# Optimization experiments

Hardware: AMD Instinct MI355X
Metric: run time of the kernel (lower is better)

## Reference

```python
import jax, jax.numpy as jnp
import numpy as np

N_NODES = 100000
N_EDGES = 1600000
DK = 32
OUT_DIM = 32


def setup_inputs() -> dict:
    key = jax.random.key(0)
    ks = jax.random.split(key, 7)
    X = jax.random.normal(ks[0], (N_NODES, DK), dtype=jnp.float32)
    K = jax.random.normal(ks[1], (N_NODES, DK), dtype=jnp.float32)
    V = jax.random.normal(ks[2], (N_NODES, DK), dtype=jnp.float32)
    # output projection (nn.Dense(out_dim)) params
    W_o = jax.random.normal(ks[3], (DK, OUT_DIM), dtype=jnp.float32) / np.sqrt(DK)
    b_o = jnp.zeros((OUT_DIM,), dtype=jnp.float32)
    # sparsity descriptor td: edge list, dst sorted so segment ops see sorted ids
    src = jax.random.randint(ks[4], (N_EDGES,), 0, N_NODES, dtype=jnp.int32)
    dst = jnp.sort(jax.random.randint(ks[5], (N_EDGES,), 0, N_NODES, dtype=jnp.int32))
    return {"X": X, "K": K, "V": V, "W_o": W_o, "b_o": b_o,
            "src": src, "dst": dst, "num_seg": N_NODES}


def reference(X, K, V, W_o, b_o, src, dst, num_seg):
    dk = X.shape[-1]
    # per-edge attention logits: <Q[dst], K[src]> / dk  -> (E,)
    scores = jnp.einsum('ed,ed->e', jnp.take(X, dst, axis=0),
                        jnp.take(K, src, axis=0)) / dk
    # segment (per-neighborhood) softmax over edges sharing a dst node
    seg_max = jax.ops.segment_max(scores, dst, num_segments=num_seg,
                                  indices_are_sorted=True)
    e = jnp.exp(scores - jnp.take(seg_max, dst))
    denom = jax.ops.segment_sum(e, dst, num_segments=num_seg,
                                indices_are_sorted=True)
    alpha = e / jnp.take(denom, dst)  # (E,)
    # weighted aggregation of values, scattered back to nodes -> (N, dk)
    agg = jax.ops.segment_sum(alpha[:, None] * jnp.take(V, src, axis=0), dst,
                              num_segments=num_seg, indices_are_sorted=True)
    # output projection W_o
    return agg @ W_o + b_o
```

## Files before the change

### kernel.cpp

```cpp
#include <hip/hip_runtime.h>
#include <math.h>

#define DK 32
#define OUT_DIM 32
#define NODES_PER_WAVE 4

__global__ void build_row_ptr_kernel(const int* __restrict__ dst, int E, int N,
                                     int* __restrict__ row_ptr) {
    int e = blockIdx.x * blockDim.x + threadIdx.x;
    if (e >= E) return;
    int cur  = dst[e];
    int prev = (e == 0) ? -1 : dst[e - 1];
    for (int j = prev + 1; j <= cur; ++j) row_ptr[j] = e;
    if (e == E - 1) {
        for (int j = cur + 1; j <= N; ++j) row_ptr[j] = E;
    }
}

__device__ __forceinline__ unsigned f2bf_rne(float x) {
    unsigned u = __float_as_uint(x);
    return (u + 0x7fffu + ((u >> 16) & 1u)) >> 16;
}

__global__ void repack_kv_kernel(const float* __restrict__ K,
                                 const float* __restrict__ V,
                                 unsigned* __restrict__ KV, int total) {
    int i = blockIdx.x * blockDim.x + threadIdx.x;
    if (i >= total) return;
    KV[i] = (f2bf_rne(V[i]) << 16) | f2bf_rne(K[i]);
}

__global__ __launch_bounds__(256) void gat_node_kv_kernel(
    const float* __restrict__ X, const uint4* __restrict__ KV,
    const float* __restrict__ Wo, const float* __restrict__ bo,
    const int* __restrict__ src, const int* __restrict__ row_ptr,
    float* __restrict__ out, int N) {

    const int tid  = threadIdx.x;
    const int wave = tid >> 6;
    const int lane = tid & 63;
    const int g    = lane >> 3;
    const int c    = lane & 7;
    const int j    = lane & 31;
    const int half = lane >> 5;

    const int n0 = (blockIdx.x * 4 + wave) * NODES_PER_WAVE;
    if (n0 >= N) return;

    float wcol[32];
#pragma unroll
    for (int k = 0; k < 32; ++k) wcol[k] = Wo[k * OUT_DIM + j];
    const float bj = bo[j];

    const float4* X4 = (const float4*)X;

    for (int i = 0; i < NODES_PER_WAVE; ++i) {
        const int n = n0 + i;
        if (n >= N) break;
        const int begin = row_ptr[n];
        const int end   = row_ptr[n + 1];

        float4 q4 = X4[n * 8 + c];
        q4.x *= 0.03125f; q4.y *= 0.03125f;
        q4.z *= 0.03125f; q4.w *= 0.03125f;

        float  l   = 0.0f;
        float4 acc = make_float4(0.0f, 0.0f, 0.0f, 0.0f);

        for (int e0 = begin; e0 < end; e0 += 16) {
            const int  ea = e0 + g;
            const int  eb = ea + 8;
            const int  sa = src[min(ea, end - 1)];
            const int  sb = src[min(eb, end - 1)];
            const uint4 A = KV[sa * 8 + c];
            const uint4 B = KV[sb * 8 + c];

            const float ka0 = __uint_as_float(A.x << 16);
            const float ka1 = __uint_as_float(A.y << 16);
            const float ka2 = __uint_as_float(A.z << 16);
            const float ka3 = __uint_as_float(A.w << 16);
            const float kb0 = __uint_as_float(B.x << 16);
            const float kb1 = __uint_as_float(B.y << 16);
            const float kb2 = __uint_as_float(B.z << 16);
            const float kb3 = __uint_as_float(B.w << 16);

            float pa = fmaf(ka0, q4.x, fmaf(ka1, q4.y, fmaf(ka2, q4.z, ka3 * q4.w)));
            float pb = fmaf(kb0, q4.x, fmaf(kb1, q4.y, fmaf(kb2, q4.z, kb3 * q4.w)));
            pa += __shfl_xor(pa, 1);  pb += __shfl_xor(pb, 1);
            pa += __shfl_xor(pa, 2);  pb += __shfl_xor(pb, 2);
            pa += __shfl_xor(pa, 4);  pb += __shfl_xor(pb, 4);

            const float wa = (ea < end) ? __expf(pa) : 0.0f;
            const float wb = (eb < end) ? __expf(pb) : 0.0f;
            l += wa + wb;

            acc.x = fmaf(wa, __uint_as_float(A.x & 0xffff0000u), acc.x);
            acc.y = fmaf(wa, __uint_as_float(A.y & 0xffff0000u), acc.y);
            acc.z = fmaf(wa, __uint_as_float(A.z & 0xffff0000u), acc.z);
            acc.w = fmaf(wa, __uint_as_float(A.w & 0xffff0000u), acc.w);
            acc.x = fmaf(wb, __uint_as_float(B.x & 0xffff0000u), acc.x);
            acc.y = fmaf(wb, __uint_as_float(B.y & 0xffff0000u), acc.y);
            acc.z = fmaf(wb, __uint_as_float(B.z & 0xffff0000u), acc.z);
            acc.w = fmaf(wb, __uint_as_float(B.w & 0xffff0000u), acc.w);
        }

#pragma unroll
        for (int m = 8; m <= 32; m <<= 1) {
            l     += __shfl_xor(l, m);
            acc.x += __shfl_xor(acc.x, m);
            acc.y += __shfl_xor(acc.y, m);
            acc.z += __shfl_xor(acc.z, m);
            acc.w += __shfl_xor(acc.w, m);
        }

        const float inv = (end > begin) ? (1.0f / l) : 0.0f;

        float ag[4] = {acc.x, acc.y, acc.z, acc.w};
        float s = 0.0f;
#pragma unroll
        for (int k = 0; k < 32; ++k) {
            const float a = __int_as_float(
                __builtin_amdgcn_readlane(__float_as_int(ag[k & 3]), k >> 2));
            s = fmaf(a, wcol[k], s);
        }
        if (half == 0) {
            out[n * OUT_DIM + j] = fmaf(s, inv, bj);
        }
    }
}

__global__ __launch_bounds__(256) void gat_node_f32_kernel(
    const float* __restrict__ X, const float* __restrict__ Km,
    const float* __restrict__ Vm, const float* __restrict__ Wo,
    const float* __restrict__ bo, const int* __restrict__ src,
    const int* __restrict__ row_ptr, float* __restrict__ out, int N) {
    const int tid  = threadIdx.x;
    const int wave = tid >> 6;
    const int lane = tid & 63;
    const int g    = lane >> 3;
    const int c    = lane & 7;
    const int j    = lane & 31;
    const int half = lane >> 5;
    const int n = blockIdx.x * 4 + wave;
    if (n >= N) return;
    const int begin = row_ptr[n];
    const int end   = row_ptr[n + 1];
    const float4* X4 = (const float4*)X;
    const float4* K4 = (const float4*)Km;
    const float4* V4 = (const float4*)Vm;
    const float4 q4 = X4[n * 8 + c];
    float  l   = 0.0f;
    float4 acc = make_float4(0.0f, 0.0f, 0.0f, 0.0f);
    for (int e0 = begin; e0 < end; e0 += 16) {
        const int  ea = e0 + g;
        const int  eb = ea + 8;
        const bool va = ea < end;
        const bool vb = eb < end;
        const int sa = src[min(ea, end - 1)];
        const int sb = src[min(eb, end - 1)];
        const float4 ka  = K4[sa * 8 + c];
        const float4 kb  = K4[sb * 8 + c];
        const float4 vva = V4[sa * 8 + c];
        const float4 vvb = V4[sb * 8 + c];
        float pa = fmaf(ka.x, q4.x, fmaf(ka.y, q4.y, fmaf(ka.z, q4.z, ka.w * q4.w)));
        float pb = fmaf(kb.x, q4.x, fmaf(kb.y, q4.y, fmaf(kb.z, q4.z, kb.w * q4.w)));
        pa += __shfl_xor(pa, 1);  pb += __shfl_xor(pb, 1);
        pa += __shfl_xor(pa, 2);  pb += __shfl_xor(pb, 2);
        pa += __shfl_xor(pa, 4);  pb += __shfl_xor(pb, 4);
        const float wa = va ? __expf(pa * 0.03125f) : 0.0f;
        const float wb = vb ? __expf(pb * 0.03125f) : 0.0f;
        l += wa + wb;
        acc.x = fmaf(wa, vva.x, acc.x);  acc.y = fmaf(wa, vva.y, acc.y);
        acc.z = fmaf(wa, vva.z, acc.z);  acc.w = fmaf(wa, vva.w, acc.w);
        acc.x = fmaf(wb, vvb.x, acc.x);  acc.y = fmaf(wb, vvb.y, acc.y);
        acc.z = fmaf(wb, vvb.z, acc.z);  acc.w = fmaf(wb, vvb.w, acc.w);
    }
#pragma unroll
    for (int m = 8; m <= 32; m <<= 1) {
        l     += __shfl_xor(l, m);
        acc.x += __shfl_xor(acc.x, m);
        acc.y += __shfl_xor(acc.y, m);
        acc.z += __shfl_xor(acc.z, m);
        acc.w += __shfl_xor(acc.w, m);
    }
    const float inv = (end > begin) ? (1.0f / l) : 0.0f;
    float ag[4] = {acc.x, acc.y, acc.z, acc.w};
    float s = 0.0f;
#pragma unroll
    for (int k = 0; k < 32; ++k) {
        const float a = __int_as_float(
            __builtin_amdgcn_readlane(__float_as_int(ag[k & 3]), k >> 2));
        s = fmaf(a, Wo[k * OUT_DIM + j], s);
    }
    if (half == 0) {
        out[n * OUT_DIM + j] = fmaf(s, inv, bo[j]);
    }
}

extern "C" void kernel_launch(void* const* d_in, const int* in_sizes, int n_in,
                              void* d_out, int out_size, void* d_ws, size_t ws_size,
                              hipStream_t stream) {
    const float* X  = (const float*)d_in[0];
    const float* Km = (const float*)d_in[1];
    const float* Vm = (const float*)d_in[2];
    const float* Wo = (const float*)d_in[3];
    const float* bo = (const float*)d_in[4];
    const int* src  = (const int*)d_in[5];
    const int* dst  = (const int*)d_in[6];

    const int N = in_sizes[0] / DK;
    const int E = in_sizes[5];

    int* row_ptr = (int*)d_ws;
    const size_t kv_off = (((size_t)(N + 1) * 4) + 127) & ~(size_t)127;
    unsigned* KV = (unsigned*)((char*)d_ws + kv_off);
    const size_t need = kv_off + (size_t)N * DK * 4;
    float* out = (float*)d_out;

    const int tb = 256;
    build_row_ptr_kernel<<<(E + tb - 1) / tb, tb, 0, stream>>>(dst, E, N, row_ptr);

    if (ws_size >= need) {
        const int total = N * DK;
        repack_kv_kernel<<<(total + tb - 1) / tb, tb, 0, stream>>>(Km, Vm, KV, total);
        const int waves = (N + NODES_PER_WAVE - 1) / NODES_PER_WAVE;
        const int grid  = (waves + 3) / 4;
        gat_node_kv_kernel<<<grid, 256, 0, stream>>>(X, (const uint4*)KV, Wo, bo,
                                                     src, row_ptr, out, N);
    } else {
        const int grid = (N + 3) / 4;
        gat_node_f32_kernel<<<grid, 256, 0, stream>>>(X, Km, Vm, Wo, bo,
                                                      src, row_ptr, out, N);
    }
}
```

Baseline: 157.8 us.

## Batch 16 nodes per wave and do output projection with bf16 MFMA

After: 151.9 us. -3.7%, faster.

```diff
diff --git a/kernel.cpp b/kernel.cpp
--- a/kernel.cpp
+++ b/kernel.cpp
@@ -3,7 +3,9 @@
 
 #define DK 32
 #define OUT_DIM 32
-#define NODES_PER_WAVE 4
+
+typedef float  f32x4  __attribute__((ext_vector_type(4)));
+typedef short  bf16x8 __attribute__((ext_vector_type(8)));
 
 __global__ void build_row_ptr_kernel(const int* __restrict__ dst, int E, int N,
                                      int* __restrict__ row_ptr) {
@@ -30,101 +32,126 @@
     KV[i] = (f2bf_rne(V[i]) << 16) | f2bf_rne(K[i]);
 }
 
-__global__ __launch_bounds__(256) void gat_node_kv_kernel(
+__global__ __launch_bounds__(256) void gat_fused_kernel(
     const float* __restrict__ X, const uint4* __restrict__ KV,
     const float* __restrict__ Wo, const float* __restrict__ bo,
     const int* __restrict__ src, const int* __restrict__ row_ptr,
     float* __restrict__ out, int N) {
+
+    __shared__ uint4 s_part[4][16 * 17];
 
     const int tid  = threadIdx.x;
     const int wave = tid >> 6;
     const int lane = tid & 63;
     const int g    = lane >> 3;
     const int c    = lane & 7;
-    const int j    = lane & 31;
-    const int half = lane >> 5;
-
-    const int n0 = (blockIdx.x * 4 + wave) * NODES_PER_WAVE;
+    const int quad = lane >> 4;
+    const int col  = lane & 15;
+
+    const int n0 = (blockIdx.x * 4 + wave) * 16;
     if (n0 >= N) return;
 
-    float wcol[32];
-#pragma unroll
-    for (int k = 0; k < 32; ++k) wcol[k] = Wo[k * OUT_DIM + j];
-    const float bj = bo[j];
+    union BF { bf16x8 v; unsigned short u[8]; };
+    BF bf0, bf1;
+#pragma unroll
+    for (int j2 = 0; j2 < 8; ++j2) {
+        bf0.u[j2] = (unsigned short)f2bf_rne(Wo[(quad * 8 + j2) * OUT_DIM + col]);
+        bf1.u[j2] = (unsigned short)f2bf_rne(Wo[(quad * 8 + j2) * OUT_DIM + 16 + col]);
+    }
+    const float bias0 = bo[col];
+    const float bias1 = bo[16 + col];
 
     const float4* X4 = (const float4*)X;
-
-    for (int i = 0; i < NODES_PER_WAVE; ++i) {
+    unsigned* part32 = (unsigned*)&s_part[wave][0];
+
+    for (int i = 0; i < 16; ++i) {
         const int n = n0 + i;
-        if (n >= N) break;
-        const int begin = row_ptr[n];
-        const int end   = row_ptr[n + 1];
-
-        float4 q4 = X4[n * 8 + c];
-        q4.x *= 0.03125f; q4.y *= 0.03125f;
-        q4.z *= 0.03125f; q4.w *= 0.03125f;
-
         float  l   = 0.0f;
         float4 acc = make_float4(0.0f, 0.0f, 0.0f, 0.0f);
-
-        for (int e0 = begin; e0 < end; e0 += 16) {
-            const int  ea = e0 + g;
-            const int  eb = ea + 8;
-            const int  sa = src[min(ea, end - 1)];
-            const int  sb = src[min(eb, end - 1)];
-            const uint4 A = KV[sa * 8 + c];
-            const uint4 B = KV[sb * 8 + c];
-
-            const float ka0 = __uint_as_float(A.x << 16);
-            const float ka1 = __uint_as_float(A.y << 16);
-            const float ka2 = __uint_as_float(A.z << 16);
-            const float ka3 = __uint_as_float(A.w << 16);
-            const float kb0 = __uint_as_float(B.x << 16);
-            const float kb1 = __uint_as_float(B.y << 16);
-            const float kb2 = __uint_as_float(B.z << 16);
-            const float kb3 = __uint_as_float(B.w << 16);
-
-            float pa = fmaf(ka0, q4.x, fmaf(ka1, q4.y, fmaf(ka2, q4.z, ka3 * q4.w)));
-            float pb = fmaf(kb0, q4.x, fmaf(kb1, q4.y, fmaf(kb2, q4.z, kb3 * q4.w)));
-            pa += __shfl_xor(pa, 1);  pb += __shfl_xor(pb, 1);
-            pa += __shfl_xor(pa, 2);  pb += __shfl_xor(pb, 2);
-            pa += __shfl_xor(pa, 4);  pb += __shfl_xor(pb, 4);
-
-            const float wa = (ea < end) ? __expf(pa) : 0.0f;
-            const float wb = (eb < end) ? __expf(pb) : 0.0f;
-            l += wa + wb;
-
-            acc.x = fmaf(wa, __uint_as_float(A.x & 0xffff0000u), acc.x);
-            acc.y = fmaf(wa, __uint_as_float(A.y & 0xffff0000u), acc.y);
-            acc.z = fmaf(wa, __uint_as_float(A.z & 0xffff0000u), acc.z);
-            acc.w = fmaf(wa, __uint_as_float(A.w & 0xffff0000u), acc.w);
-            acc.x = fmaf(wb, __uint_as_float(B.x & 0xffff0000u), acc.x);
-            acc.y = fmaf(wb, __uint_as_float(B.y & 0xffff0000u), acc.y);
-            acc.z = fmaf(wb, __uint_as_float(B.z & 0xffff0000u), acc.z);
-            acc.w = fmaf(wb, __uint_as_float(B.w & 0xffff0000u), acc.w);
+        int begin = 0, end = 0;
+
+        if (n < N) {
+            begin = row_ptr[n];
+            end   = row_ptr[n + 1];
+
+            float4 q4 = X4[n * 8 + c];
+            q4.x *= 0.03125f; q4.y *= 0.03125f;
+            q4.z *= 0.03125f; q4.w *= 0.03125f;
+
+            for (int e0 = begin; e0 < end; e0 += 16) {
+                const int ea = e0 + g;
+                const int eb = ea + 8;
+                const int sa = src[min(ea, end - 1)];
+                const int sb = src[min(eb, end - 1)];
+                const uint4 A = KV[sa * 8 + c];
+                const uint4 B = KV[sb * 8 + c];
+
+                const float ka0 = __uint_as_float(A.x << 16);
+                const float ka1 = __uint_as_float(A.y << 16);
+                const float ka2 = __uint_as_float(A.z << 16);
+                const float ka3 = __uint_as_float(A.w << 16);
+                const float kb0 = __uint_as_float(B.x << 16);
+                const float kb1 = __uint_as_float(B.y << 16);
+                const float kb2 = __uint_as_float(B.z << 16);
+                const float kb3 = __uint_as_float(B.w << 16);
+
+                float pa = fmaf(ka0, q4.x, fmaf(ka1, q4.y, fmaf(ka2, q4.z, ka3 * q4.w)));
+                float pb = fmaf(kb0, q4.x, fmaf(kb1, q4.y, fmaf(kb2, q4.z, kb3 * q4.w)));
+                pa += __shfl_xor(pa, 1);  pb += __shfl_xor(pb, 1);
+                pa += __shfl_xor(pa, 2);  pb += __shfl_xor(pb, 2);
+                pa += __shfl_xor(pa, 4);  pb += __shfl_xor(pb, 4);
+
+                const float wa = (ea < end) ? __expf(pa) : 0.0f;
+                const float wb = (eb < end) ? __expf(pb) : 0.0f;
+                l += wa + wb;
+
+                acc.x = fmaf(wa, __uint_as_float(A.x & 0xffff0000u), acc.x);
+                acc.y = fmaf(wa, __uint_as_float(A.y & 0xffff0000u), acc.y);
+                acc.z = fmaf(wa, __uint_as_float(A.z & 0xffff0000u), acc.z);
+                acc.w = fmaf(wa, __uint_as_float(A.w & 0xffff0000u), acc.w);
+                acc.x = fmaf(wb, __uint_as_float(B.x & 0xffff0000u), acc.x);
+                acc.y = fmaf(wb, __uint_as_float(B.y & 0xffff0000u), acc.y);
+                acc.z = fmaf(wb, __uint_as_float(B.z & 0xffff0000u), acc.z);
+                acc.w = fmaf(wb, __uint_as_float(B.w & 0xffff0000u), acc.w);
+            }
         }
 
-#pragma unroll
-        for (int m = 8; m <= 32; m <<= 1) {
-            l     += __shfl_xor(l, m);
-            acc.x += __shfl_xor(acc.x, m);
-            acc.y += __shfl_xor(acc.y, m);
-            acc.z += __shfl_xor(acc.z, m);
-            acc.w += __shfl_xor(acc.w, m);
+        l     += __shfl_xor(l, 8);
+        acc.x += __shfl_xor(acc.x, 8);
+        acc.y += __shfl_xor(acc.y, 8);
+        acc.z += __shfl_xor(acc.z, 8);
+        acc.w += __shfl_xor(acc.w, 8);
+        l += __shfl_xor(l, 16);
+        l += __shfl_xor(l, 32);
+
+        const float inv = (end > begin) ? (1.0f / l) : 0.0f;
+        acc.x *= inv; acc.y *= inv; acc.z *= inv; acc.w *= inv;
+
+        if ((g & 1) == 0) {
+            const int p   = g >> 1;
+            const int off = i * 68 + p * 16 + c * 2;
+            part32[off]     = f2bf_rne(acc.x) | (f2bf_rne(acc.y) << 16);
+            part32[off + 1] = f2bf_rne(acc.z) | (f2bf_rne(acc.w) << 16);
         }
-
-        const float inv = (end > begin) ? (1.0f / l) : 0.0f;
-
-        float ag[4] = {acc.x, acc.y, acc.z, acc.w};
-        float s = 0.0f;
-#pragma unroll
-        for (int k = 0; k < 32; ++k) {
-            const float a = __int_as_float(
-                __builtin_amdgcn_readlane(__float_as_int(ag[k & 3]), k >> 2));
-            s = fmaf(a, wcol[k], s);
-        }
-        if (half == 0) {
-            out[n * OUT_DIM + j] = fmaf(s, inv, bj);
+    }
+
+    union AF { uint4 u; bf16x8 v; };
+    f32x4 C0 = {bias0, bias0, bias0, bias0};
+    f32x4 C1 = {bias1, bias1, bias1, bias1};
+#pragma unroll
+    for (int cc = 0; cc < 4; ++cc) {
+        AF a;
+        a.u = s_part[wave][col * 17 + cc * 4 + quad];
+        C0 = __builtin_amdgcn_mfma_f32_16x16x32_bf16(a.v, bf0.v, C0, 0, 0, 0);
+        C1 = __builtin_amdgcn_mfma_f32_16x16x32_bf16(a.v, bf1.v, C1, 0, 0, 0);
+    }
+
+#pragma unroll
+    for (int r = 0; r < 4; ++r) {
+        const int n = n0 + quad * 4 + r;
+        if (n < N) {
+            out[n * OUT_DIM + col]      = C0[r];
+            out[n * OUT_DIM + 16 + col] = C1[r];
         }
     }
 }
@@ -223,10 +250,10 @@
     if (ws_size >= need) {
         const int total = N * DK;
         repack_kv_kernel<<<(total + tb - 1) / tb, tb, 0, stream>>>(Km, Vm, KV, total);
-        const int waves = (N + NODES_PER_WAVE - 1) / NODES_PER_WAVE;
+        const int waves = (N + 15) / 16;
         const int grid  = (waves + 3) / 4;
-        gat_node_kv_kernel<<<grid, 256, 0, stream>>>(X, (const uint4*)KV, Wo, bo,
-                                                     src, row_ptr, out, N);
+        gat_fused_kernel<<<grid, 256, 0, stream>>>(X, (const uint4*)KV, Wo, bo,
+                                                   src, row_ptr, out, N);
     } else {
         const int grid = (N + 3) / 4;
         gat_node_f32_kernel<<<grid, 256, 0, stream>>>(X, Km, Vm, Wo, bo,
```
